# Kernel tuning notes

Hardware: AMD Instinct MI355X
Metric: run time of the kernel (lower is better)

## Reference

```python
import jax, jax.numpy as jnp
import numpy as np

B, T, E, C, H = 8, 96, 96, 256, 8
D = C // H
HID = int(C * 4.0)
EPS = 1e-5


def _ln(x, g, b):
    m = x.mean(-1, keepdims=True)
    v = ((x - m) ** 2).mean(-1, keepdims=True)
    return (x - m) * jax.lax.rsqrt(v + EPS) * g + b


def setup_inputs() -> dict:
    key = jax.random.key(0)
    ks = jax.random.split(key, 20)
    s = 0.02
    inp = {
        "x": jax.random.normal(ks[0], (B, T, E, C), jnp.float32),
        "adj_mask": jax.random.uniform(ks[1], (E, E), jnp.float32) * 2.0 - 1.0,  # direction cosines in [-1,1]
        "n1_g": jnp.ones((C,)), "n1_b": jnp.zeros((C,)),
        "s_wq": jax.random.normal(ks[2], (C, C)) * s,
        "s_wk": jax.random.normal(ks[3], (C, C)) * s,
        "s_wv": jax.random.normal(ks[4], (C, C)) * s,
        "s_wp": jax.random.normal(ks[5], (C, C)) * s,
        "s_bp": jnp.zeros((C,)),
        "s_ng": jnp.ones((C,)), "s_nb": jnp.zeros((C,)),
        "s_gamma": jax.random.normal(ks[6], (1,)) * 0.1,
        "n2_g": jnp.ones((C,)), "n2_b": jnp.zeros((C,)),
        "t_wq": jax.random.normal(ks[7], (C, C)) * s,
        "t_wk": jax.random.normal(ks[8], (C, C)) * s,
        "t_wv": jax.random.normal(ks[9], (C, C)) * s,
        "t_wp": jax.random.normal(ks[10], (C, C)) * s,
        "t_bp": jnp.zeros((C,)),
        "t_gamma": jax.random.normal(ks[11], (1,)) * 0.1,
        "n3_g": jnp.ones((C,)), "n3_b": jnp.zeros((C,)),
        "m_w1": jax.random.normal(ks[12], (C, HID)) * s,
        "m_b1": jnp.zeros((HID,)),
        "m_w2": jax.random.normal(ks[13], (HID, C)) * s,
        "m_b2": jnp.zeros((C,)),
    }
    return inp


def _interp_linear_T(x, t_new):
    # x: [B, T, E, C]; torch F.interpolate(mode='linear', align_corners=False) over T
    t = x.shape[1]
    scale = t / t_new
    src = (jnp.arange(t_new, dtype=jnp.float32) + 0.5) * scale - 0.5
    src = jnp.clip(src, 0.0, t - 1)
    i0 = jnp.floor(src).astype(jnp.int32)
    i1 = jnp.minimum(i0 + 1, t - 1)
    w = (src - i0.astype(jnp.float32))[None, :, None, None]
    return x[:, i0] * (1.0 - w) + x[:, i1] * w


def reference(x, adj_mask, n1_g, n1_b, s_wq, s_wk, s_wv, s_wp, s_bp, s_ng, s_nb, s_gamma,
              n2_g, n2_b, t_wq, t_wk, t_wv, t_wp, t_bp, t_gamma,
              n3_g, n3_b, m_w1, m_b1, m_w2, m_b2):
    b, t, e, c = x.shape
    h, d = H, C // H

    # ---- spatial geometric-cosine attention (per frame) ----
    xs = _ln(x, n1_g, n1_b)                                    # identity inside spatial_attn
    q = (xs @ s_wq).reshape(b, t, e, h, d)
    k = (xs @ s_wk).reshape(b, t, e, h, d)
    v = (xs @ s_wv).reshape(b, t, e, h, d)
    attn = jnp.einsum('btqhd,btkhd->bthqk', q, k)
    attn = (attn * adj_mask + 1.0) * 0.5                        # masked-cosine, no softmax
    o = jnp.einsum('bthqk,btkhd->btqhd', attn, v).reshape(b, t, e, c)
    o = _ln(o @ s_wp + s_bp, s_ng, s_nb)
    x = x + (xs + s_gamma * o)

    # ---- temporal softmax attention (per edge) ----
    xt = _ln(x, n2_g, n2_b)
    q = (xt @ t_wq).reshape(b, t, e, h, d)
    k = (xt @ t_wk).reshape(b, t, e, h, d)
    v = (xt @ t_wv).reshape(b, t, e, h, d)
    attn = jnp.einsum('bqehd,bkehd->behqk', q, k) * (d ** -0.5)
    attn = jax.nn.softmax(attn, axis=-1)
    o = jnp.einsum('behqk,bkehd->bqehd', attn, v).reshape(b, t, e, c)
    o = o @ t_wp + t_bp
    x = x + t_gamma * o

    # ---- MLP ----
    xm = _ln(x, n3_g, n3_b)
    x = x + (jax.nn.gelu(xm @ m_w1 + m_b1, approximate=False) @ m_w2 + m_b2)

    # ---- temporal downsampling (interpolate) ----
    t_new = t // 2 + t % 2
    if t > 1:
        x = _interp_linear_T(x, t_new)
    return x
```

## Files before the change

kernel.cpp:

```cpp
#include <hip/hip_runtime.h>
#include <cmath>

constexpr int BB = 8, TT = 96, EE = 96, CC = 256, HHD = 8, DDm = 32;
constexpr int NTOK = BB * TT * EE;
constexpr int TOUT = TT / 2;

typedef unsigned short u16;
typedef short bf16x8 __attribute__((ext_vector_type(8)));
typedef float f32x4 __attribute__((ext_vector_type(4)));

__device__ __forceinline__ float bf2f(u16 u) {
  union { unsigned int i; float f; } v; v.i = ((unsigned int)u) << 16; return v.f;
}
__device__ __forceinline__ u16 f2bf(float f) {
  union { unsigned int i; float f; } v; v.f = f;
  return (u16)((v.i + 0x7FFFu + ((v.i >> 16) & 1u)) >> 16);
}
__device__ __forceinline__ float wsum(float v) {
#pragma unroll
  for (int off = 32; off; off >>= 1) v += __shfl_xor(v, off);
  return v;
}
__device__ __forceinline__ float gelu_f(float x) {
  return 0.5f * x * (1.0f + erff(x * 0.70710678118654752f));
}
__device__ __forceinline__ int remap_row(int row, int mode) {
  if (mode == 0) return row;
  int b = row / (TT * EE);
  int rem = row - b * (TT * EE);
  if (mode == 1) { int t = rem / EE, e = rem - t * EE; return (b * EE + e) * TT + t; }
  int e = rem / TT, t = rem - e * TT;
  return (b * TT + t) * EE + e;
}

struct WPtr8 { const float* p[8]; };
__global__ void k_transpose8(WPtr8 src, u16* __restrict__ dst) {
  const float* in = src.p[blockIdx.y];
  u16* out = dst + (size_t)blockIdx.y * 65536;
  int idx = blockIdx.x * 256 + threadIdx.x;
  int k = idx >> 8, c = idx & 255;
  out[c * 256 + k] = f2bf(in[idx]);
}

__global__ void k_transpose(const float* __restrict__ in, u16* __restrict__ out, int K, int Nc, int n) {
  int idx = blockIdx.x * 256 + threadIdx.x;
  if (idx < n) {
    int k = idx / Nc, c = idx - k * Nc;
    out[c * K + k] = f2bf(in[idx]);
  }
}

__global__ void k_cvt(const float* __restrict__ in, u16* __restrict__ out, int n) {
  int idx = blockIdx.x * 256 + threadIdx.x;
  if (idx < n) out[idx] = f2bf(in[idx]);
}

__global__ __launch_bounds__(256) void k_ln_in(const float* __restrict__ x,
                                               u16* __restrict__ A, const float* __restrict__ g,
                                               const float* __restrict__ b) {
  int wv = threadIdx.x >> 6, lane = threadIdx.x & 63;
  long tok = (long)blockIdx.x * 4 + wv;
  int c = lane * 4;
  long off = tok * CC + c;
  float4 v = *(const float4*)(x + off);
  float s = v.x + v.y + v.z + v.w;
  float sq = v.x * v.x + v.y * v.y + v.z * v.z + v.w * v.w;
  s = wsum(s); sq = wsum(sq);
  float m = s * (1.0f / CC);
  float rs = rsqrtf(sq * (1.0f / CC) - m * m + 1e-5f);
  float4 gv = *(const float4*)(g + c);
  float4 bv = *(const float4*)(b + c);
  ushort4 o;
  o.x = f2bf((v.x - m) * rs * gv.x + bv.x);
  o.y = f2bf((v.y - m) * rs * gv.y + bv.y);
  o.z = f2bf((v.z - m) * rs * gv.z + bv.z);
  o.w = f2bf((v.w - m) * rs * gv.w + bv.w);
  *(ushort4*)(A + off) = o;
}

__global__ __launch_bounds__(256) void k_ln_f32(const float* __restrict__ X, u16* __restrict__ A,
                                                const float* __restrict__ g, const float* __restrict__ b) {
  int wv = threadIdx.x >> 6, lane = threadIdx.x & 63;
  long tok = (long)blockIdx.x * 4 + wv;
  int c = lane * 4;
  long off = tok * CC + c;
  float4 v = *(const float4*)(X + off);
  float s = v.x + v.y + v.z + v.w;
  float sq = v.x * v.x + v.y * v.y + v.z * v.z + v.w * v.w;
  s = wsum(s); sq = wsum(sq);
  float m = s * (1.0f / CC);
  float rs = rsqrtf(sq * (1.0f / CC) - m * m + 1e-5f);
  float4 gv = *(const float4*)(g + c);
  float4 bv = *(const float4*)(b + c);
  ushort4 o;
  o.x = f2bf((v.x - m) * rs * gv.x + bv.x);
  o.y = f2bf((v.y - m) * rs * gv.y + bv.y);
  o.z = f2bf((v.z - m) * rs * gv.z + bv.z);
  o.w = f2bf((v.w - m) * rs * gv.w + bv.w);
  *(ushort4*)(A + off) = o;
}

__global__ __launch_bounds__(256) void k_sp_combine(const float* __restrict__ xin, float* __restrict__ X,
                                                    u16* __restrict__ A, const u16* __restrict__ P,
                                                    const float* __restrict__ n1g, const float* __restrict__ n1b,
                                                    const float* __restrict__ sg,
                                                    const float* __restrict__ s_ng, const float* __restrict__ s_nb,
                                                    const float* __restrict__ n2g, const float* __restrict__ n2b) {
  int wv = threadIdx.x >> 6, lane = threadIdx.x & 63;
  long tok = (long)blockIdx.x * 4 + wv;
  int c = lane * 4;
  long off = tok * CC + c;
  float4 xv = *(const float4*)(xin + off);
  float s1 = xv.x + xv.y + xv.z + xv.w;
  float q1 = xv.x * xv.x + xv.y * xv.y + xv.z * xv.z + xv.w * xv.w;
  s1 = wsum(s1); q1 = wsum(q1);
  float m1 = s1 * (1.0f / CC);
  float r1 = rsqrtf(q1 * (1.0f / CC) - m1 * m1 + 1e-5f);
  float4 g1 = *(const float4*)(n1g + c);
  float4 b1 = *(const float4*)(n1b + c);
  float xs0 = (xv.x - m1) * r1 * g1.x + b1.x;
  float xs1 = (xv.y - m1) * r1 * g1.y + b1.y;
  float xs2 = (xv.z - m1) * r1 * g1.z + b1.z;
  float xs3 = (xv.w - m1) * r1 * g1.w + b1.w;
  ushort4 up = *(const ushort4*)(P + off);
  float4 p = make_float4(bf2f(up.x), bf2f(up.y), bf2f(up.z), bf2f(up.w));
  float s = p.x + p.y + p.z + p.w;
  float sq = p.x * p.x + p.y * p.y + p.z * p.z + p.w * p.w;
  s = wsum(s); sq = wsum(sq);
  float m = s * (1.0f / CC);
  float rs = rsqrtf(sq * (1.0f / CC) - m * m + 1e-5f);
  float4 ug = *(const float4*)(s_ng + c);
  float4 ub = *(const float4*)(s_nb + c);
  float o0 = (p.x - m) * rs * ug.x + ub.x;
  float o1 = (p.y - m) * rs * ug.y + ub.y;
  float o2 = (p.z - m) * rs * ug.z + ub.z;
  float o3 = (p.w - m) * rs * ug.w + ub.w;
  float gsg = sg[0];
  float x0 = xv.x + xs0 + gsg * o0;
  float x1 = xv.y + xs1 + gsg * o1;
  float x2 = xv.z + xs2 + gsg * o2;
  float x3 = xv.w + xs3 + gsg * o3;
  *(float4*)(X + off) = make_float4(x0, x1, x2, x3);
  float s2 = x0 + x1 + x2 + x3;
  float sq2 = x0 * x0 + x1 * x1 + x2 * x2 + x3 * x3;
  s2 = wsum(s2); sq2 = wsum(sq2);
  float m2 = s2 * (1.0f / CC);
  float rs2 = rsqrtf(sq2 * (1.0f / CC) - m2 * m2 + 1e-5f);
  float4 g2 = *(const float4*)(n2g + c);
  float4 b2 = *(const float4*)(n2b + c);
  ushort4 o;
  o.x = f2bf((x0 - m2) * rs2 * g2.x + b2.x);
  o.y = f2bf((x1 - m2) * rs2 * g2.y + b2.y);
  o.z = f2bf((x2 - m2) * rs2 * g2.z + b2.z);
  o.w = f2bf((x3 - m2) * rs2 * g2.w + b2.w);
  *(ushort4*)(A + off) = o;
}

__global__ __launch_bounds__(256) void k_gemm128(const u16* __restrict__ act, const u16* __restrict__ Wt,
                                                 const float* __restrict__ bias, const float* __restrict__ gptr,
                                                 u16* __restrict__ outB, float* __restrict__ Xacc,
                                                 int Kd, int Nc, int lda, int ldb, int epi, int remap) {
  __shared__ __align__(16) u16 smem[3 * 8192];
  int gx = gridDim.x;
  int nwg = gx * gridDim.y;
  int lid = blockIdx.y * gx + blockIdx.x;
  if ((nwg & 7) == 0) lid = (lid & 7) * (nwg >> 3) + (lid >> 3);
  int m0 = (lid / gx) * 128, n0 = (lid % gx) * 128;
  int tid = threadIdx.x;
  int wv = tid >> 6, lane = tid & 63, lm = lane & 15, quad = lane >> 4;
  int wr = wv >> 1, wc = wv & 1;
  f32x4 acc[4][4];
#pragma unroll
  for (int i = 0; i < 4; i++)
#pragma unroll
    for (int j = 0; j < 4; j++) acc[i][j] = (f32x4){0.f, 0.f, 0.f, 0.f};

  int srow = tid >> 2;
  int sseg = (tid & 3) ^ ((srow >> 1) & 3);
  const u16* pa = act + (long)(m0 + srow) * lda + sseg * 8;
  const u16* pb = Wt + (long)(n0 + srow) * ldb + sseg * 8;

  auto STAGE = [&](int buf, int kk) {
    u16* sb = smem + buf * 8192;
#pragma unroll
    for (int j = 0; j < 2; j++) {
      __builtin_amdgcn_global_load_lds(pa + (long)j * 64 * lda + kk, sb + (j * 256 + wv * 64) * 8, 16, 0, 0);
      __builtin_amdgcn_global_load_lds(pb + (long)j * 64 * ldb + kk, sb + 4096 + (j * 256 + wv * 64) * 8, 16, 0, 0);
    }
  };

  int nsteps = Kd >> 5;
  STAGE(0, 0);
  STAGE(1, 32);
  asm volatile("s_waitcnt vmcnt(4)" ::: "memory");
  __builtin_amdgcn_sched_barrier(0);
  __builtin_amdgcn_s_barrier();

  int xsw = (lm >> 1) & 3;
  int cur = 0;
  for (int t = 0; t < nsteps; ++t) {
    if (t + 2 < nsteps) {
      int nb = cur + 2; if (nb >= 3) nb -= 3;
      STAGE(nb, (t + 2) << 5);
    }
    const u16* As = smem + cur * 8192;
    const u16* Bs = As + 4096;
    bf16x8 af[4], bfv[4];
#pragma unroll
    for (int q = 0; q < 4; q++) {
      af[q] = *(const bf16x8*)&As[(wr * 64 + q * 16 + lm) * 32 + (quad ^ xsw) * 8];
      bfv[q] = *(const bf16x8*)&Bs[(wc * 64 + q * 16 + lm) * 32 + (quad ^ xsw) * 8];
    }
    __builtin_amdgcn_s_setprio(1);
#pragma unroll
    for (int ti = 0; ti < 4; ti++)
#pragma unroll
      for (int tj = 0; tj < 4; tj++)
        acc[ti][tj] = __builtin_amdgcn_mfma_f32_16x16x32_bf16(af[ti], bfv[tj], acc[ti][tj], 0, 0, 0);
    __builtin_amdgcn_s_setprio(0);
    asm volatile("s_waitcnt lgkmcnt(0)" ::: "memory");
    __builtin_amdgcn_sched_barrier(0);
    if (t + 2 < nsteps) asm volatile("s_waitcnt vmcnt(4)" ::: "memory");
    else                asm volatile("s_waitcnt vmcnt(0)" ::: "memory");
    __builtin_amdgcn_sched_barrier(0);
    __builtin_amdgcn_s_barrier();
    cur += 1; if (cur >= 3) cur -= 3;
  }

  if (epi == 3) {
    float gm = gptr ? gptr[0] : 1.0f;
    float* fs = (float*)smem;
#pragma unroll
    for (int half = 0; half < 2; half++) {
      if (half) __syncthreads();
      if (wr == half) {
#pragma unroll
        for (int tj = 0; tj < 4; tj++) {
          int col = wc * 64 + tj * 16 + lm;
          float bv = bias ? bias[n0 + col] : 0.0f;
#pragma unroll
          for (int ti = 0; ti < 4; ti++)
#pragma unroll
            for (int r = 0; r < 4; r++)
              fs[(ti * 16 + quad * 4 + r) * 132 + col] = gm * (acc[ti][tj][r] + bv);
        }
      }
      __syncthreads();
#pragma unroll
      for (int p = 0; p < 8; p++) {
        int idx = p * 256 + tid;
        int row = idx >> 5, c4 = idx & 31;
        int grow = remap_row(m0 + half * 64 + row, remap);
        float* gp = Xacc + (long)grow * Nc + n0 + c4 * 4;
        float4 xv = *(float4*)gp;
        float4 sv = *(const float4*)&fs[row * 132 + c4 * 4];
        xv.x += sv.x; xv.y += sv.y; xv.z += sv.z; xv.w += sv.w;
        *(float4*)gp = xv;
      }
    }
  } else {
#pragma unroll
    for (int tj = 0; tj < 4; tj++) {
      int col = wc * 64 + tj * 16 + lm;
      float bv = (epi >= 1 && bias) ? bias[n0 + col] : 0.0f;
#pragma unroll
      for (int ti = 0; ti < 4; ti++)
#pragma unroll
        for (int r = 0; r < 4; r++) {
          float vv = acc[ti][tj][r] + bv;
          if (epi == 2) vv = gelu_f(vv);
          smem[(wr * 64 + ti * 16 + quad * 4 + r) * 136 + col] = f2bf(vv);
        }
    }
    __syncthreads();
#pragma unroll
    for (int p = 0; p < 8; p++) {
      int idx = p * 256 + tid;
      int row = idx >> 4, c8 = idx & 15;
      int grow = remap_row(m0 + row, remap);
      *(uint4*)(outB + (long)grow * Nc + n0 + c8 * 8) = *(const uint4*)&smem[row * 136 + c8 * 8];
    }
  }
}

__global__ __launch_bounds__(384) void k_sp_attn(const u16* __restrict__ QKV, const u16* __restrict__ adj,
                                                 u16* __restrict__ O) {
  __shared__ __align__(16) u16 Qs[96 * 32];
  __shared__ __align__(16) u16 Ks[96 * 32];
  __shared__ __align__(16) u16 Vt[32 * 104];
  __shared__ __align__(16) u16 Ss[96 * 104];
  int blk = blockIdx.x;
  blk = (blk & 7) * ((int)gridDim.x >> 3) + (blk >> 3);
  int h = blk & 7, t = (blk >> 3) % TT, b = blk / (8 * TT);
  long base = ((long)(b * TT + t) * EE) * 768 + h * DDm;
  int tid = threadIdx.x;
  {
    int row = tid >> 2, seg = tid & 3;
    long goff = base + (long)row * 768 + seg * 8;
    *(uint4*)&Qs[row * 32 + seg * 8] = *(const uint4*)(QKV + goff);
    *(uint4*)&Ks[row * 32 + seg * 8] = *(const uint4*)(QKV + goff + 256);
    union { uint4 u; u16 s[8]; } vv;
    vv.u = *(const uint4*)(QKV + goff + 512);
#pragma unroll
    for (int i = 0; i < 8; i++) Vt[(seg * 8 + i) * 104 + row] = vv.s[i];
    int cb = seg * 24;
#pragma unroll
    for (int i = 0; i < 3; i++)
      *(uint4*)&Ss[row * 104 + cb + i * 8] = *(const uint4*)(adj + row * 96 + cb + i * 8);
  }
  __syncthreads();
  int wv = tid >> 6, lane = tid & 63, lm = lane & 15, quad = lane >> 4;
  bf16x8 aq = *(const bf16x8*)&Qs[(wv * 16 + lm) * 32 + quad * 8];
  f32x4 sc[6];
#pragma unroll
  for (int j = 0; j < 6; j++) {
    bf16x8 bk = *(const bf16x8*)&Ks[(j * 16 + lm) * 32 + quad * 8];
    f32x4 z = (f32x4){0.f, 0.f, 0.f, 0.f};
    sc[j] = __builtin_amdgcn_mfma_f32_16x16x32_bf16(aq, bk, z, 0, 0, 0);
  }
  u16 sv[6][4];
#pragma unroll
  for (int j = 0; j < 6; j++) {
    int col = j * 16 + lm;
#pragma unroll
    for (int r = 0; r < 4; r++) {
      int row = wv * 16 + quad * 4 + r;
      float a = bf2f(Ss[row * 104 + col]);
      sv[j][r] = f2bf((sc[j][r] * a + 1.0f) * 0.5f);
    }
  }
  __syncthreads();
#pragma unroll
  for (int j = 0; j < 6; j++) {
    int col = j * 16 + lm;
#pragma unroll
    for (int r = 0; r < 4; r++) Ss[(wv * 16 + quad * 4 + r) * 104 + col] = sv[j][r];
  }
  __syncthreads();
  f32x4 oc[2];
  oc[0] = (f32x4){0.f, 0.f, 0.f, 0.f};
  oc[1] = (f32x4){0.f, 0.f, 0.f, 0.f};
#pragma unroll
  for (int ks = 0; ks < 3; ks++) {
    bf16x8 as = *(const bf16x8*)&Ss[(wv * 16 + lm) * 104 + ks * 32 + quad * 8];
#pragma unroll
    for (int n = 0; n < 2; n++) {
      bf16x8 bv = *(const bf16x8*)&Vt[(n * 16 + lm) * 104 + ks * 32 + quad * 8];
      oc[n] = __builtin_amdgcn_mfma_f32_16x16x32_bf16(as, bv, oc[n], 0, 0, 0);
    }
  }
  long obase = ((long)(b * TT + t) * EE) * CC + h * DDm;
#pragma unroll
  for (int n = 0; n < 2; n++)
#pragma unroll
    for (int r = 0; r < 4; r++) {
      int row = wv * 16 + quad * 4 + r;
      O[obase + (long)row * CC + n * 16 + lm] = f2bf(oc[n][r]);
    }
}

__global__ __launch_bounds__(384) void k_tp_attn(const u16* __restrict__ QKV, u16* __restrict__ O) {
  __shared__ __align__(16) u16 Qs[96 * 32];
  __shared__ __align__(16) u16 Ks[96 * 32];
  __shared__ __align__(16) u16 Vt[32 * 104];
  __shared__ __align__(16) u16 Ss[96 * 104];
  int blk = blockIdx.x;
  blk = (blk & 7) * ((int)gridDim.x >> 3) + (blk >> 3);
  int h = blk & 7, e = (blk >> 3) % EE, b = blk / (8 * EE);
  long base = ((long)(b * EE + e) * TT) * 768 + h * DDm;
  int tid = threadIdx.x;
  {
    int row = tid >> 2, seg = tid & 3;
    long goff = base + (long)row * 768 + seg * 8;
    *(uint4*)&Qs[row * 32 + seg * 8] = *(const uint4*)(QKV + goff);
    *(uint4*)&Ks[row * 32 + seg * 8] = *(const uint4*)(QKV + goff + 256);
    union { uint4 u; u16 s[8]; } vv;
    vv.u = *(const uint4*)(QKV + goff + 512);
#pragma unroll
    for (int i = 0; i < 8; i++) Vt[(seg * 8 + i) * 104 + row] = vv.s[i];
  }
  __syncthreads();
  int wv = tid >> 6, lane = tid & 63, lm = lane & 15, quad = lane >> 4;
  bf16x8 aq = *(const bf16x8*)&Qs[(wv * 16 + lm) * 32 + quad * 8];
  f32x4 sc[6];
#pragma unroll
  for (int j = 0; j < 6; j++) {
    bf16x8 bk = *(const bf16x8*)&Ks[(j * 16 + lm) * 32 + quad * 8];
    f32x4 z = (f32x4){0.f, 0.f, 0.f, 0.f};
    sc[j] = __builtin_amdgcn_mfma_f32_16x16x32_bf16(aq, bk, z, 0, 0, 0);
  }
  const float scale = 0.17677669529663687f;
#pragma unroll
  for (int r = 0; r < 4; r++) {
    float mx = -1e30f;
#pragma unroll
    for (int j = 0; j < 6; j++) { sc[j][r] *= scale; mx = fmaxf(mx, sc[j][r]); }
#pragma unroll
    for (int mask = 1; mask < 16; mask <<= 1) mx = fmaxf(mx, __shfl_xor(mx, mask));
    float sum = 0.f;
#pragma unroll
    for (int j = 0; j < 6; j++) { float p = __expf(sc[j][r] - mx); sc[j][r] = p; sum += p; }
#pragma unroll
    for (int mask = 1; mask < 16; mask <<= 1) sum += __shfl_xor(sum, mask);
    float inv = 1.0f / sum;
#pragma unroll
    for (int j = 0; j < 6; j++) sc[j][r] *= inv;
  }
#pragma unroll
  for (int j = 0; j < 6; j++) {
    int col = j * 16 + lm;
#pragma unroll
    for (int r = 0; r < 4; r++) Ss[(wv * 16 + quad * 4 + r) * 104 + col] = f2bf(sc[j][r]);
  }
  __syncthreads();
  f32x4 oc[2];
  oc[0] = (f32x4){0.f, 0.f, 0.f, 0.f};
  oc[1] = (f32x4){0.f, 0.f, 0.f, 0.f};
#pragma unroll
  for (int ks = 0; ks < 3; ks++) {
    bf16x8 as = *(const bf16x8*)&Ss[(wv * 16 + lm) * 104 + ks * 32 + quad * 8];
#pragma unroll
    for (int n = 0; n < 2; n++) {
      bf16x8 bv = *(const bf16x8*)&Vt[(n * 16 + lm) * 104 + ks * 32 + quad * 8];
      oc[n] = __builtin_amdgcn_mfma_f32_16x16x32_bf16(as, bv, oc[n], 0, 0, 0);
    }
  }
  long obase = ((long)(b * EE + e) * TT) * CC + h * DDm;
#pragma unroll
  for (int n = 0; n < 2; n++)
#pragma unroll
    for (int r = 0; r < 4; r++) {
      int row = wv * 16 + quad * 4 + r;
      O[obase + (long)row * CC + n * 16 + lm] = f2bf(oc[n][r]);
    }
}

__global__ __launch_bounds__(256) void k_down(const float* __restrict__ X, float* __restrict__ out) {
  long i4 = ((long)blockIdx.x * 256 + threadIdx.x) * 4;
  long tmp = i4;
  int c = (int)(tmp & 255); tmp >>= 8;
  int e = (int)(tmp % EE); tmp /= EE;
  int i = (int)(tmp % TOUT);
  int b = (int)(tmp / TOUT);
  long src0 = (((long)b * TT + 2 * i) * EE + e) * CC + c;
  float4 a = *(const float4*)(X + src0);
  float4 bb = *(const float4*)(X + src0 + (long)EE * CC);
  float4 o = make_float4(0.5f * (a.x + bb.x), 0.5f * (a.y + bb.y),
                         0.5f * (a.z + bb.z), 0.5f * (a.w + bb.w));
  *(float4*)(out + i4) = o;
}

extern "C" void kernel_launch(void* const* d_in, const int* in_sizes, int n_in,
                              void* d_out, int out_size, void* d_ws, size_t ws_size,
                              hipStream_t stream) {
  (void)in_sizes; (void)n_in; (void)out_size; (void)ws_size;
  const float* x   = (const float*)d_in[0];
  const float* adj = (const float*)d_in[1];
  const float* n1g = (const float*)d_in[2];
  const float* n1b = (const float*)d_in[3];
  const float* swq = (const float*)d_in[4];
  const float* swk = (const float*)d_in[5];
  const float* swv = (const float*)d_in[6];
  const float* swp = (const float*)d_in[7];
  const float* sbp = (const float*)d_in[8];
  const float* sng = (const float*)d_in[9];
  const float* snb = (const float*)d_in[10];
  const float* sg  = (const float*)d_in[11];
  const float* n2g = (const float*)d_in[12];
  const float* n2b = (const float*)d_in[13];
  const float* twq = (const float*)d_in[14];
  const float* twk = (const float*)d_in[15];
  const float* twv = (const float*)d_in[16];
  const float* twp = (const float*)d_in[17];
  const float* tbp = (const float*)d_in[18];
  const float* tg  = (const float*)d_in[19];
  const float* n3g = (const float*)d_in[20];
  const float* n3b = (const float*)d_in[21];
  const float* mw1 = (const float*)d_in[22];
  const float* mb1 = (const float*)d_in[23];
  const float* mw2 = (const float*)d_in[24];
  const float* mb2 = (const float*)d_in[25];
  float* out = (float*)d_out;

  size_t nc = (size_t)NTOK * CC;
  float* X  = (float*)d_ws;
  u16* A    = (u16*)(X + nc);
  u16* QKV  = A + nc;
  u16* Pb   = QKV;
  u16* Hh   = QKV;
  u16* wts  = QKV + 3 * nc;
  u16* swq_t = wts;
  u16* swp_t = wts + 3 * 65536;
  u16* twq_t = wts + 4 * 65536;
  u16* twp_t = wts + 7 * 65536;
  u16* w1_t  = wts + 8 * 65536;
  u16* w2_t  = w1_t + 262144;
  u16* adj_b = w2_t + 262144;

  WPtr8 w8; w8.p[0] = swq; w8.p[1] = swk; w8.p[2] = swv; w8.p[3] = swp;
  w8.p[4] = twq; w8.p[5] = twk; w8.p[6] = twv; w8.p[7] = twp;
  k_transpose8<<<dim3(256, 8), 256, 0, stream>>>(w8, wts);
  k_transpose<<<(256 * 1024 + 255) / 256, 256, 0, stream>>>(mw1, w1_t, 256, 1024, 256 * 1024);
  k_transpose<<<(1024 * 256 + 255) / 256, 256, 0, stream>>>(mw2, w2_t, 1024, 256, 1024 * 256);
  k_cvt<<<(EE * EE + 255) / 256, 256, 0, stream>>>(adj, adj_b, EE * EE);

  auto gemm = [&](const u16* act, const u16* Wt, const float* bias, const float* gamma,
                  u16* outB, float* Xacc, int Kd, int Nc, int lda, int ldb, int epi, int remap, int M) {
    dim3 g(Nc / 128, M / 128);
    k_gemm128<<<g, 256, 0, stream>>>(act, Wt, bias, gamma, outB, Xacc, Kd, Nc, lda, ldb, epi, remap);
  };

  int lnBlocks = NTOK / 4;

  k_ln_in<<<lnBlocks, 256, 0, stream>>>(x, A, n1g, n1b);
  gemm(A, swq_t, nullptr, nullptr, QKV, nullptr, 256, 768, 256, 256, 0, 0, NTOK);
  k_sp_attn<<<BB * TT * HHD, 384, 0, stream>>>(QKV, adj_b, A);
  gemm(A, swp_t, sbp, nullptr, Pb, nullptr, 256, 256, 256, 256, 1, 0, NTOK);
  k_sp_combine<<<lnBlocks, 256, 0, stream>>>(x, X, A, Pb, n1g, n1b, sg, sng, snb, n2g, n2b);

  gemm(A, twq_t, nullptr, nullptr, QKV, nullptr, 256, 768, 256, 256, 0, 1, NTOK);
  k_tp_attn<<<BB * EE * HHD, 384, 0, stream>>>(QKV, A);
  gemm(A, twp_t, tbp, tg, nullptr, X, 256, 256, 256, 256, 3, 2, NTOK);

  k_ln_f32<<<lnBlocks, 256, 0, stream>>>(X, A, n3g, n3b);
  for (int hf = 0; hf < 2; hf++) {
    long r0 = (long)hf * (NTOK / 2);
    gemm(A + r0 * CC, w1_t, mb1, nullptr, Hh, nullptr, 256, 1024, 256, 256, 2, 0, NTOK / 2);
    gemm(Hh, w2_t, mb2, nullptr, nullptr, X + r0 * CC, 1024, 256, 1024, 1024, 3, 0, NTOK / 2);
  }

  long outElems = (long)BB * TOUT * EE * CC;
  k_down<<<(int)(outElems / 4 / 256), 256, 0, stream>>>(X, out);
}
```

Baseline: 672.6 us.

## Process all heads per attention block with register prefetch of next head

Spatial and temporal attention kernels now loop over all 8 heads inside one block instead of launching one block per head, cutting the grid by 8x. The next head's Q/K/V slices are loaded into registers while the current head computes, to overlap global loads with MFMA work. This trades parallelism and occupancy (fewer blocks, extra barriers per head) for fewer launches and better latency hiding within a block.

```diff
diff --git a/kernel.cpp b/kernel.cpp
--- a/kernel.cpp
+++ b/kernel.cpp
@@ -291,72 +291,82 @@
   __shared__ __align__(16) u16 Ss[96 * 104];
   int blk = blockIdx.x;
   blk = (blk & 7) * ((int)gridDim.x >> 3) + (blk >> 3);
-  int h = blk & 7, t = (blk >> 3) % TT, b = blk / (8 * TT);
-  long base = ((long)(b * TT + t) * EE) * 768 + h * DDm;
+  int t = blk % TT, b = blk / TT;
+  long fQ = ((long)(b * TT + t) * EE) * 768;
+  long fO = ((long)(b * TT + t) * EE) * CC;
   int tid = threadIdx.x;
-  {
-    int row = tid >> 2, seg = tid & 3;
-    long goff = base + (long)row * 768 + seg * 8;
-    *(uint4*)&Qs[row * 32 + seg * 8] = *(const uint4*)(QKV + goff);
-    *(uint4*)&Ks[row * 32 + seg * 8] = *(const uint4*)(QKV + goff + 256);
-    union { uint4 u; u16 s[8]; } vv;
-    vv.u = *(const uint4*)(QKV + goff + 512);
-#pragma unroll
-    for (int i = 0; i < 8; i++) Vt[(seg * 8 + i) * 104 + row] = vv.s[i];
-    int cb = seg * 24;
+  int row = tid >> 2, seg = tid & 3;
+  int wv = tid >> 6, lane = tid & 63, lm = lane & 15, quad = lane >> 4;
+  long gq0 = fQ + (long)row * 768 + seg * 8;
+  uint4 rq = *(const uint4*)(QKV + gq0);
+  uint4 rk = *(const uint4*)(QKV + gq0 + 256);
+  uint4 rv = *(const uint4*)(QKV + gq0 + 512);
+  int cb = seg * 24;
+  for (int h = 0; h < 8; ++h) {
+    *(uint4*)&Qs[row * 32 + seg * 8] = rq;
+    *(uint4*)&Ks[row * 32 + seg * 8] = rk;
+    { union { uint4 u; u16 s[8]; } vv; vv.u = rv;
+#pragma unroll
+      for (int i = 0; i < 8; i++) Vt[(seg * 8 + i) * 104 + row] = vv.s[i]; }
 #pragma unroll
     for (int i = 0; i < 3; i++)
       *(uint4*)&Ss[row * 104 + cb + i * 8] = *(const uint4*)(adj + row * 96 + cb + i * 8);
+    __syncthreads();
+    if (h < 7) {
+      long g = gq0 + (h + 1) * 32;
+      rq = *(const uint4*)(QKV + g);
+      rk = *(const uint4*)(QKV + g + 256);
+      rv = *(const uint4*)(QKV + g + 512);
+      __builtin_amdgcn_sched_barrier(0);
+    }
+    bf16x8 aq = *(const bf16x8*)&Qs[(wv * 16 + lm) * 32 + quad * 8];
+    f32x4 sc[6];
+#pragma unroll
+    for (int j = 0; j < 6; j++) {
+      bf16x8 bk = *(const bf16x8*)&Ks[(j * 16 + lm) * 32 + quad * 8];
+      f32x4 z = (f32x4){0.f, 0.f, 0.f, 0.f};
+      sc[j] = __builtin_amdgcn_mfma_f32_16x16x32_bf16(aq, bk, z, 0, 0, 0);
+    }
+    u16 sv[6][4];
+#pragma unroll
+    for (int j = 0; j < 6; j++) {
+      int col = j * 16 + lm;
+#pragma unroll
+      for (int r = 0; r < 4; r++) {
+        int rrow = wv * 16 + quad * 4 + r;
+        float a = bf2f(Ss[rrow * 104 + col]);
+        sv[j][r] = f2bf((sc[j][r] * a + 1.0f) * 0.5f);
+      }
+    }
+    __syncthreads();
+#pragma unroll
+    for (int j = 0; j < 6; j++) {
+      int col = j * 16 + lm;
+#pragma unroll
+      for (int r = 0; r < 4; r++) Ss[(wv * 16 + quad * 4 + r) * 104 + col] = sv[j][r];
+    }
+    __syncthreads();
+    f32x4 oc[2];
+    oc[0] = (f32x4){0.f, 0.f, 0.f, 0.f};
+    oc[1] = (f32x4){0.f, 0.f, 0.f, 0.f};
+#pragma unroll
+    for (int ks = 0; ks < 3; ks++) {
+      bf16x8 as = *(const bf16x8*)&Ss[(wv * 16 + lm) * 104 + ks * 32 + quad * 8];
+#pragma unroll
+      for (int n = 0; n < 2; n++) {
+        bf16x8 bv = *(const bf16x8*)&Vt[(n * 16 + lm) * 104 + ks * 32 + quad * 8];
+        oc[n] = __builtin_amdgcn_mfma_f32_16x16x32_bf16(as, bv, oc[n], 0, 0, 0);
+      }
+    }
+#pragma unroll
+    for (int n = 0; n < 2; n++)
+#pragma unroll
+      for (int r = 0; r < 4; r++) {
+        int rrow = wv * 16 + quad * 4 + r;
+        O[fO + (long)rrow * CC + h * DDm + n * 16 + lm] = f2bf(oc[n][r]);
+      }
+    __syncthreads();
   }
-  __syncthreads();
-  int wv = tid >> 6, lane = tid & 63, lm = lane & 15, quad = lane >> 4;
-  bf16x8 aq = *(const bf16x8*)&Qs[(wv * 16 + lm) * 32 + quad * 8];
-  f32x4 sc[6];
-#pragma unroll
-  for (int j = 0; j < 6; j++) {
-    bf16x8 bk = *(const bf16x8*)&Ks[(j * 16 + lm) * 32 + quad * 8];
-    f32x4 z = (f32x4){0.f, 0.f, 0.f, 0.f};
-    sc[j] = __builtin_amdgcn_mfma_f32_16x16x32_bf16(aq, bk, z, 0, 0, 0);
-  }
-  u16 sv[6][4];
-#pragma unroll
-  for (int j = 0; j < 6; j++) {
-    int col = j * 16 + lm;
-#pragma unroll
-    for (int r = 0; r < 4; r++) {
-      int row = wv * 16 + quad * 4 + r;
-      float a = bf2f(Ss[row * 104 + col]);
-      sv[j][r] = f2bf((sc[j][r] * a + 1.0f) * 0.5f);
-    }
-  }
-  __syncthreads();
-#pragma unroll
-  for (int j = 0; j < 6; j++) {
-    int col = j * 16 + lm;
-#pragma unroll
-    for (int r = 0; r < 4; r++) Ss[(wv * 16 + quad * 4 + r) * 104 + col] = sv[j][r];
-  }
-  __syncthreads();
-  f32x4 oc[2];
-  oc[0] = (f32x4){0.f, 0.f, 0.f, 0.f};
-  oc[1] = (f32x4){0.f, 0.f, 0.f, 0.f};
-#pragma unroll
-  for (int ks = 0; ks < 3; ks++) {
-    bf16x8 as = *(const bf16x8*)&Ss[(wv * 16 + lm) * 104 + ks * 32 + quad * 8];
-#pragma unroll
-    for (int n = 0; n < 2; n++) {
-      bf16x8 bv = *(const bf16x8*)&Vt[(n * 16 + lm) * 104 + ks * 32 + quad * 8];
-      oc[n] = __builtin_amdgcn_mfma_f32_16x16x32_bf16(as, bv, oc[n], 0, 0, 0);
-    }
-  }
-  long obase = ((long)(b * TT + t) * EE) * CC + h * DDm;
-#pragma unroll
-  for (int n = 0; n < 2; n++)
-#pragma unroll
-    for (int r = 0; r < 4; r++) {
-      int row = wv * 16 + quad * 4 + r;
-      O[obase + (long)row * CC + n * 16 + lm] = f2bf(oc[n][r]);
-    }
 }
 
 __global__ __launch_bounds__(384) void k_tp_attn(const u16* __restrict__ QKV, u16* __restrict__ O) {
@@ -366,73 +376,83 @@
   __shared__ __align__(16) u16 Ss[96 * 104];
   int blk = blockIdx.x;
   blk = (blk & 7) * ((int)gridDim.x >> 3) + (blk >> 3);
-  int h = blk & 7, e = (blk >> 3) % EE, b = blk / (8 * EE);
-  long base = ((long)(b * EE + e) * TT) * 768 + h * DDm;
+  int e = blk % EE, b = blk / EE;
+  long fQ = ((long)(b * EE + e) * TT) * 768;
+  long fO = ((long)(b * EE + e) * TT) * CC;
   int tid = threadIdx.x;
-  {
-    int row = tid >> 2, seg = tid & 3;
-    long goff = base + (long)row * 768 + seg * 8;
-    *(uint4*)&Qs[row * 32 + seg * 8] = *(const uint4*)(QKV + goff);
-    *(uint4*)&Ks[row * 32 + seg * 8] = *(const uint4*)(QKV + goff + 256);
-    union { uint4 u; u16 s[8]; } vv;
-    vv.u = *(const uint4*)(QKV + goff + 512);
-#pragma unroll
-    for (int i = 0; i < 8; i++) Vt[(seg * 8 + i) * 104 + row] = vv.s[i];
+  int row = tid >> 2, seg = tid & 3;
+  int wv = tid >> 6, lane = tid & 63, lm = lane & 15, quad = lane >> 4;
+  long gq0 = fQ + (long)row * 768 + seg * 8;
+  uint4 rq = *(const uint4*)(QKV + gq0);
+  uint4 rk = *(const uint4*)(QKV + gq0 + 256);
+  uint4 rv = *(const uint4*)(QKV + gq0 + 512);
+  const float scale = 0.17677669529663687f;
+  for (int h = 0; h < 8; ++h) {
+    *(uint4*)&Qs[row * 32 + seg * 8] = rq;
+    *(uint4*)&Ks[row * 32 + seg * 8] = rk;
+    { union { uint4 u; u16 s[8]; } vv; vv.u = rv;
+#pragma unroll
+      for (int i = 0; i < 8; i++) Vt[(seg * 8 + i) * 104 + row] = vv.s[i]; }
+    __syncthreads();
+    if (h < 7) {
+      long g = gq0 + (h + 1) * 32;
+      rq = *(const uint4*)(QKV + g);
+      rk = *(const uint4*)(QKV + g + 256);
+      rv = *(const uint4*)(QKV + g + 512);
+      __builtin_amdgcn_sched_barrier(0);
+    }
+    bf16x8 aq = *(const bf16x8*)&Qs[(wv * 16 + lm) * 32 + quad * 8];
+    f32x4 sc[6];
+#pragma unroll
+    for (int j = 0; j < 6; j++) {
+      bf16x8 bk = *(const bf16x8*)&Ks[(j * 16 + lm) * 32 + quad * 8];
+      f32x4 z = (f32x4){0.f, 0.f, 0.f, 0.f};
+      sc[j] = __builtin_amdgcn_mfma_f32_16x16x32_bf16(aq, bk, z, 0, 0, 0);
+    }
+#pragma unroll
+    for (int r = 0; r < 4; r++) {
+      float mx = -1e30f;
+#pragma unroll
+      for (int j = 0; j < 6; j++) { sc[j][r] *= scale; mx = fmaxf(mx, sc[j][r]); }
+#pragma unroll
+      for (int mask = 1; mask < 16; mask <<= 1) mx = fmaxf(mx, __shfl_xor(mx, mask));
+      float sum = 0.f;
+#pragma unroll
+      for (int j = 0; j < 6; j++) { float p = __expf(sc[j][r] - mx); sc[j][r] = p; sum += p; }
+#pragma unroll
+      for (int mask = 1; mask < 16; mask <<= 1) sum += __shfl_xor(sum, mask);
+      float inv = 1.0f / sum;
+#pragma unroll
+      for (int j = 0; j < 6; j++) sc[j][r] *= inv;
+    }
+#pragma unroll
+    for (int j = 0; j < 6; j++) {
+      int col = j * 16 + lm;
+#pragma unroll
+      for (int r = 0; r < 4; r++) Ss[(wv * 16 + quad * 4 + r) * 104 + col] = f2bf(sc[j][r]);
+    }
+    __syncthreads();
+    f32x4 oc[2];
+    oc[0] = (f32x4){0.f, 0.f, 0.f, 0.f};
+    oc[1] = (f32x4){0.f, 0.f, 0.f, 0.f};
+#pragma unroll
+    for (int ks = 0; ks < 3; ks++) {
+      bf16x8 as = *(const bf16x8*)&Ss[(wv * 16 + lm) * 104 + ks * 32 + quad * 8];
+#pragma unroll
+      for (int n = 0; n < 2; n++) {
+        bf16x8 bv = *(const bf16x8*)&Vt[(n * 16 + lm) * 104 + ks * 32 + quad * 8];
+        oc[n] = __builtin_amdgcn_mfma_f32_16x16x32_bf16(as, bv, oc[n], 0, 0, 0);
+      }
+    }
+#pragma unroll
+    for (int n = 0; n < 2; n++)
+#pragma unroll
+      for (int r = 0; r < 4; r++) {
+        int rrow = wv * 16 + quad * 4 + r;
+        O[fO + (long)rrow * CC + h * DDm + n * 16 + lm] = f2bf(oc[n][r]);
+      }
+    __syncthreads();
   }
-  __syncthreads();
-  int wv = tid >> 6, lane = tid & 63, lm = lane & 15, quad = lane >> 4;
-  bf16x8 aq = *(const bf16x8*)&Qs[(wv * 16 + lm) * 32 + quad * 8];
-  f32x4 sc[6];
-#pragma unroll
-  for (int j = 0; j < 6; j++) {
-    bf16x8 bk = *(const bf16x8*)&Ks[(j * 16 + lm) * 32 + quad * 8];
-    f32x4 z = (f32x4){0.f, 0.f, 0.f, 0.f};
-    sc[j] = __builtin_amdgcn_mfma_f32_16x16x32_bf16(aq, bk, z, 0, 0, 0);
-  }
-  const float scale = 0.17677669529663687f;
-#pragma unroll
-  for (int r = 0; r < 4; r++) {
-    float mx = -1e30f;
-#pragma unroll
-    for (int j = 0; j < 6; j++) { sc[j][r] *= scale; mx = fmaxf(mx, sc[j][r]); }
-#pragma unroll
-    for (int mask = 1; mask < 16; mask <<= 1) mx = fmaxf(mx, __shfl_xor(mx, mask));
-    float sum = 0.f;
-#pragma unroll
-    for (int j = 0; j < 6; j++) { float p = __expf(sc[j][r] - mx); sc[j][r] = p; sum += p; }
-#pragma unroll
-    for (int mask = 1; mask < 16; mask <<= 1) sum += __shfl_xor(sum, mask);
-    float inv = 1.0f / sum;
-#pragma unroll
-    for (int j = 0; j < 6; j++) sc[j][r] *= inv;
-  }
-#pragma unroll
-  for (int j = 0; j < 6; j++) {
-    int col = j * 16 + lm;
-#pragma unroll
-    for (int r = 0; r < 4; r++) Ss[(wv * 16 + quad * 4 + r) * 104 + col] = f2bf(sc[j][r]);
-  }
-  __syncthreads();
-  f32x4 oc[2];
-  oc[0] = (f32x4){0.f, 0.f, 0.f, 0.f};
-  oc[1] = (f32x4){0.f, 0.f, 0.f, 0.f};
-#pragma unroll
-  for (int ks = 0; ks < 3; ks++) {
-    bf16x8 as = *(const bf16x8*)&Ss[(wv * 16 + lm) * 104 + ks * 32 + quad * 8];
-#pragma unroll
-    for (int n = 0; n < 2; n++) {
-      bf16x8 bv = *(const bf16x8*)&Vt[(n * 16 + lm) * 104 + ks * 32 + quad * 8];
-      oc[n] = __builtin_amdgcn_mfma_f32_16x16x32_bf16(as, bv, oc[n], 0, 0, 0);
-    }
-  }
-  long obase = ((long)(b * EE + e) * TT) * CC + h * DDm;
-#pragma unroll
-  for (int n = 0; n < 2; n++)
-#pragma unroll
-    for (int r = 0; r < 4; r++) {
-      int row = wv * 16 + quad * 4 + r;
-      O[obase + (long)row * CC + n * 16 + lm] = f2bf(oc[n][r]);
-    }
 }
 
 __global__ __launch_bounds__(256) void k_down(const float* __restrict__ X, float* __restrict__ out) {
@@ -514,12 +534,12 @@
 
   k_ln_in<<<lnBlocks, 256, 0, stream>>>(x, A, n1g, n1b);
   gemm(A, swq_t, nullptr, nullptr, QKV, nullptr, 256, 768, 256, 256, 0, 0, NTOK);
-  k_sp_attn<<<BB * TT * HHD, 384, 0, stream>>>(QKV, adj_b, A);
+  k_sp_attn<<<BB * TT, 384, 0, stream>>>(QKV, adj_b, A);
   gemm(A, swp_t, sbp, nullptr, Pb, nullptr, 256, 256, 256, 256, 1, 0, NTOK);
   k_sp_combine<<<lnBlocks, 256, 0, stream>>>(x, X, A, Pb, n1g, n1b, sg, sng, snb, n2g, n2b);
 
   gemm(A, twq_t, nullptr, nullptr, QKV, nullptr, 256, 768, 256, 256, 0, 1, NTOK);
-  k_tp_attn<<<BB * EE * HHD, 384, 0, stream>>>(QKV, A);
+  k_tp_attn<<<BB * EE, 384, 0, stream>>>(QKV, A);
   gemm(A, twp_t, tbp, tg, nullptr, X, 256, 256, 256, 256, 3, 2, NTOK);
 
   k_ln_f32<<<lnBlocks, 256, 0, stream>>>(X, A, n3g, n3b);
```

Measured after the change: 699.7 us (median of 3 runs). +4.0%, slower.
